# Kernel tuning notes

Measured on AMD Instinct MI355X. Metric: run time of the kernel, lower is better.

The kernel has to match this reference:

```python
import jax, jax.numpy as jnp
import numpy as np

# ---- constants mirroring init_kwargs ----
S = 128          # sheet_units
KA = 25          # aff_cf_units
C = 2            # aff_cf_channels
KL = 25          # lat_cf_units
EXC = 9          # exc_units
DA = 1           # aff_cf_dilation
DL = 1           # lat_cf_dilation
HOMEO_TARGET = 0.04
STRENGTH = 1.0

# ---- radial helper masks (get_circle / get_radial_cos) ----
def _dist(n):
    g = jnp.arange(n, dtype=jnp.float32) - (n - 1) / 2.0
    return jnp.sqrt(g[:, None] ** 2 + g[None, :] ** 2)

def _circle(n, r):
    return (_dist(n) < r).astype(jnp.float32)

def _rcos(n, wl):
    return jnp.cos(_dist(n) * jnp.pi / wl)

# afferent envelope: [C*KA*KA], channel-major like torch repeat+view
_ae = _rcos(KA, KA) ** 2 * _circle(KA, KA / 2)
_ae = _ae / _ae.max()
AFF_ENV = jnp.tile(_ae.reshape(1, KA * KA), (C, 1)).reshape(C * KA * KA)

# lateral (LRI) envelope: [KL*KL]
_inh = _rcos(KL, EXC / DL) ** 2 * _circle(KL, EXC / (2 * DL))
_le = _rcos(KL, KL) ** 2 * (1.0 - _inh) * _circle(KL, KL / 2)
LRI_ENV = (_le / _le.max()).reshape(KL * KL)

def _unfold(x, k, dil):
    """x: [C,H,W] -> patches [L, C*k*k], torch F.unfold ordering (C slowest)."""
    Cc, H, W = x.shape
    out = H - dil * (k - 1)
    idx = jnp.arange(out)[:, None] + dil * jnp.arange(k)[None, :]  # [out,k]
    p = x[:, idx, :]          # [C,out,k,W]
    p = p[:, :, :, idx]       # [C,out,k,out,k]
    p = p.transpose(1, 3, 0, 2, 4)  # [out_i,out_j,C,ki,kj]
    return p.reshape(out * out, Cc * k * k)

def setup_inputs() -> dict:
    key = jax.random.key(0)
    k1, k2 = jax.random.split(key)
    in_size = S + DA * (KA - 1)  # 152
    x = jax.random.uniform(k1, (1, C, in_size, in_size), dtype=jnp.float32)
    rfs = jax.random.uniform(k2, (S * S, C * KA * KA, 1), dtype=jnp.float32)
    rfs = rfs / rfs.sum(1, keepdims=True)
    lat_weights = jnp.ones((S * S, KL * KL, 1), jnp.float32) / (KL * KL)
    adathresh = jnp.zeros((1, 1, S, S), jnp.float32)
    return {"x": x, "rfs": rfs, "lat_weights": lat_weights, "adathresh": adathresh}

def _forward(x, rfs, lat_weights, adathresh):
    relu = jax.nn.relu
    rfs = relu(rfs)                 # no_grad positive clamp of params
    lw = relu(lat_weights)
    # afferent: unfold + envelope + per-pixel dot (bmm with [L,F,1])
    tiles = _unfold(x[0], KA, DA) * AFF_ENV[None, :]          # [L, C*KA*KA]
    raw_aff = jnp.einsum('lf,lf->l', tiles, rfs[:, :, 0]).reshape(S, S)
    aff = jax.lax.stop_gradient(raw_aff) - adathresh[0, 0]
    lat = relu(aff)
    # lateral inhibition: pad so unfold yields S*S positions
    p = DL * (KL - 1) // 2
    lt = _unfold(jnp.pad(lat, p)[None], KL, DL) * LRI_ENV[None, :]  # [L, KL*KL]
    lat_neg = jnp.einsum('lf,lf->l', lt, jax.lax.stop_gradient(lw)[:, :, 0]).reshape(S, S)
    lat = lat - lat_neg
    lat = jnp.tanh(relu(lat * STRENGTH + aff))
    # hebbian lateral correlations term (learning_flag path)
    lt2 = _unfold(jnp.pad(lat, p, constant_values=HOMEO_TARGET)[None], KL, DL) * LRI_ENV[None, :]
    weighted = lt2 * lat.reshape(S * S, 1)
    lat_correlations = jnp.einsum('lf,lf->', weighted, lw[:, :, 0])
    return (raw_aff.reshape(1, 1, S, S), lat.reshape(1, 1, S, S),
            lat_correlations, tiles[:, None, :])

def reference(x, rfs, lat_weights, adathresh):
    return _forward(x, rfs, lat_weights, adathresh)
```

## Files before the change

kernel.cpp:

```cpp
#include <hip/hip_runtime.h>
#include <math.h>

#define S 128
#define KA 25
#define KL 25
#define PATCH (KA * KA)
#define FEAT (2 * PATCH)
#define PI_F 3.14159265358979323846f

#define WS_ENV 0
#define WS_LAT0 640
#define WS_PART 17024

__global__ __launch_bounds__(256) void k_tiles_aff(const float* __restrict__ x,
                                                   const float* __restrict__ rfs,
                                                   const float* __restrict__ ada,
                                                   float* __restrict__ raw_aff,
                                                   float* __restrict__ tiles,
                                                   float* __restrict__ ws) {
    __shared__ float s_ae[PATCH];
    __shared__ float s_part[4];
    const int tid = threadIdx.x;
    const int lane = tid & 63;
    const int wv = tid >> 6;

    for (int i = tid; i < PATCH; i += 256) {
        float di = (float)(i / KA) - 12.0f;
        float dj = (float)(i % KA) - 12.0f;
        float d = sqrtf(di * di + dj * dj);
        float v = 0.0f;
        if (d < 12.5f) {
            float c = cosf(d * (PI_F / 25.0f));
            v = c * c;
        }
        s_ae[i] = v;
    }
    __syncthreads();

    const int l = blockIdx.x;
    const int li = l >> 7;
    const int lj = l & 127;
    const long base = (long)l * FEAT;

    float acc = 0.0f;
    for (int f = tid; f < FEAT; f += 256) {
        int c = (f >= PATCH) ? 1 : 0;
        int r = f - c * PATCH;
        int ki = r / KA;
        int kj = r - ki * KA;
        float xv = x[c * (152 * 152) + (li + ki) * 152 + (lj + kj)];
        float t = xv * s_ae[r];
        tiles[base + f] = t;
        acc += t * fmaxf(rfs[base + f], 0.0f);
    }

    for (int off = 32; off > 0; off >>= 1) acc += __shfl_down(acc, off);
    if (lane == 0) s_part[wv] = acc;
    __syncthreads();
    if (tid == 0) {
        float ra = s_part[0] + s_part[1] + s_part[2] + s_part[3];
        raw_aff[l] = ra;
        ws[WS_LAT0 + l] = fmaxf(ra - ada[l], 0.0f);
    }

    if (blockIdx.x == 0) {
        __syncthreads();
        float m = 0.0f;
        for (int i = tid; i < PATCH; i += 256) {
            float di = (float)(i / KL) - 12.0f;
            float dj = (float)(i % KL) - 12.0f;
            float d = sqrtf(di * di + dj * dj);
            float v = 0.0f;
            if (d < 12.5f) {
                float c1 = cosf(d * (PI_F / 25.0f));
                float inh = 0.0f;
                if (d < 4.5f) {
                    float c2 = cosf(d * (PI_F / 9.0f));
                    inh = c2 * c2;
                }
                v = c1 * c1 * (1.0f - inh);
            }
            s_ae[i] = v;
            m = fmaxf(m, v);
        }
        for (int off = 32; off > 0; off >>= 1) m = fmaxf(m, __shfl_down(m, off));
        if (lane == 0) s_part[wv] = m;
        __syncthreads();
        float inv = 1.0f / fmaxf(fmaxf(s_part[0], s_part[1]),
                                 fmaxf(s_part[2], s_part[3]));
        for (int i = tid; i < PATCH; i += 256) ws[WS_ENV + i] = s_ae[i] * inv;
    }
}

__global__ __launch_bounds__(256) void k_lat(const float* __restrict__ raw_aff,
                                             const float* __restrict__ ada,
                                             const float* __restrict__ lw,
                                             float* __restrict__ latf,
                                             const float* __restrict__ ws) {
    __shared__ float s_le[PATCH];
    const int tid = threadIdx.x;
    for (int i = tid; i < PATCH; i += 256) s_le[i] = ws[WS_ENV + i];
    __syncthreads();

    const int lane = tid & 63;
    const int wv = tid >> 6;
    const int l = blockIdx.x * 4 + wv;
    const int li = l >> 7;
    const int lj = l & 127;
    const long base = (long)l * PATCH;
    const float* __restrict__ lat0 = ws + WS_LAT0;

    float acc = 0.0f;
    for (int f = lane; f < PATCH; f += 64) {
        int ki = f / KL;
        int kj = f - ki * KL;
        int ri = li + ki - 12;
        int rj = lj + kj - 12;
        float lv = 0.0f;
        if (ri >= 0 && ri < S && rj >= 0 && rj < S) lv = lat0[ri * S + rj];
        acc += lv * s_le[f] * fmaxf(lw[base + f], 0.0f);
    }
    for (int off = 32; off > 0; off >>= 1) acc += __shfl_down(acc, off);

    if (lane == 0) {
        float aff_l = raw_aff[l] - ada[l];
        float lat0_l = fmaxf(aff_l, 0.0f);
        float v = (lat0_l - acc)  + aff_l;
        latf[l] = tanhf(fmaxf(v, 0.0f));
    }
}

__global__ __launch_bounds__(256) void k_corr(const float* __restrict__ latf,
                                              const float* __restrict__ lw,
                                              float* __restrict__ ws) {
    __shared__ float s_le[PATCH];
    __shared__ float s_part[4];
    const int tid = threadIdx.x;
    for (int i = tid; i < PATCH; i += 256) s_le[i] = ws[WS_ENV + i];
    __syncthreads();

    const int lane = tid & 63;
    const int wv = tid >> 6;
    const int l = blockIdx.x * 4 + wv;
    const int li = l >> 7;
    const int lj = l & 127;
    const long base = (long)l * PATCH;

    float acc = 0.0f;
    for (int f = lane; f < PATCH; f += 64) {
        int ki = f / KL;
        int kj = f - ki * KL;
        int ri = li + ki - 12;
        int rj = lj + kj - 12;
        float lv = 0.04f;
        if (ri >= 0 && ri < S && rj >= 0 && rj < S) lv = latf[ri * S + rj];
        acc += lv * s_le[f] * fmaxf(lw[base + f], 0.0f);
    }
    for (int off = 32; off > 0; off >>= 1) acc += __shfl_down(acc, off);

    if (lane == 0) s_part[wv] = acc * latf[l];
    __syncthreads();
    if (tid == 0)
        ws[WS_PART + blockIdx.x] = s_part[0] + s_part[1] + s_part[2] + s_part[3];
}

__global__ __launch_bounds__(256) void k_reduce(const float* __restrict__ ws,
                                                float* __restrict__ corr) {
    __shared__ float s_part[4];
    const int tid = threadIdx.x;
    const int lane = tid & 63;
    const int wv = tid >> 6;
    float acc = 0.0f;
    for (int i = tid; i < 4096; i += 256) acc += ws[WS_PART + i];
    for (int off = 32; off > 0; off >>= 1) acc += __shfl_down(acc, off);
    if (lane == 0) s_part[wv] = acc;
    __syncthreads();
    if (tid == 0) corr[0] = s_part[0] + s_part[1] + s_part[2] + s_part[3];
}

extern "C" void kernel_launch(void* const* d_in, const int* in_sizes, int n_in,
                              void* d_out, int out_size, void* d_ws, size_t ws_size,
                              hipStream_t stream) {
    const float* x   = (const float*)d_in[0];
    const float* rfs = (const float*)d_in[1];
    const float* lw  = (const float*)d_in[2];
    const float* ada = (const float*)d_in[3];

    float* out      = (float*)d_out;
    float* raw_aff  = out;
    float* latf     = out + S * S;
    float* corr     = out + 2 * S * S;
    float* tiles    = out + 2 * S * S + 1;
    float* ws       = (float*)d_ws;

    k_tiles_aff<<<S * S, 256, 0, stream>>>(x, rfs, ada, raw_aff, tiles, ws);
    k_lat<<<(S * S) / 4, 256, 0, stream>>>(raw_aff, ada, lw, latf, ws);
    k_corr<<<(S * S) / 4, 256, 0, stream>>>(latf, lw, ws);
    k_reduce<<<1, 256, 0, stream>>>(ws, corr);
}
```

Measured before the change: 229.7 us.

## Split tile output into vectorized kernel, pad lateral maps, vectorize weight loads

Moves the large tiles output write into its own grid-stride kernel that emits aligned float4 stores, and makes the afferent dot-product kernel read rfs as float4 with peel and tail handling. Precomputes both envelopes once in an init kernel, and writes the lateral activity maps into zero- and 0.04-padded 152x152 buffers so the lateral and correlation passes need no bounds checks. Those passes also read lw as float4. The cost is that x is read twice, through two kernel launches, and the padded buffers are re-initialized on every call.

```diff
diff --git a/kernel.cpp b/kernel.cpp
--- a/kernel.cpp
+++ b/kernel.cpp
@@ -4,91 +4,175 @@
 #define S 128
 #define KA 25
 #define KL 25
-#define PATCH (KA * KA)
-#define FEAT (2 * PATCH)
+#define PATCH 625
+#define FEAT 1250
 #define PI_F 3.14159265358979323846f
-
-#define WS_ENV 0
-#define WS_LAT0 640
-#define WS_PART 17024
-
-__global__ __launch_bounds__(256) void k_tiles_aff(const float* __restrict__ x,
-                                                   const float* __restrict__ rfs,
-                                                   const float* __restrict__ ada,
-                                                   float* __restrict__ raw_aff,
-                                                   float* __restrict__ tiles,
-                                                   float* __restrict__ ws) {
-    __shared__ float s_ae[PATCH];
+#define PADW 152
+#define PADA (PADW * PADW)
+
+#define WS_LRI 0
+#define WS_AE 640
+#define WS_LAT0P 1280
+#define WS_LATFP 24384
+#define WS_PART 47488
+
+__device__ __forceinline__ int div25(int r) { return (r * 10486) >> 18; }
+
+__device__ __forceinline__ int woff(int r) { return r + 127 * div25(r); }
+
+__global__ __launch_bounds__(256) void k_init(float* __restrict__ ws) {
+    const int tid = threadIdx.x;
+    if (blockIdx.x == 0) {
+        __shared__ float s_tmp[640];
+        __shared__ float s_red[4];
+        for (int s = tid; s < 640; s += 256) {
+            int q = s / 160;
+            int t = s - q * 160;
+            int r = (t << 2) | q;
+            float v = 0.0f;
+            if (r < PATCH) {
+                float di = (float)div25(r) - 12.0f;
+                float dj = (float)(r - 25 * div25(r)) - 12.0f;
+                float d = sqrtf(di * di + dj * dj);
+                if (d < 12.5f) {
+                    float c = cosf(d * (PI_F / 25.0f));
+                    v = c * c;
+                }
+            }
+            ws[WS_AE + s] = v;
+        }
+        float m = 0.0f;
+        for (int s = tid; s < 640; s += 256) {
+            int q = s / 160;
+            int t = s - q * 160;
+            int r = (t << 2) | q;
+            float v = 0.0f;
+            if (r < PATCH) {
+                float di = (float)div25(r) - 12.0f;
+                float dj = (float)(r - 25 * div25(r)) - 12.0f;
+                float d = sqrtf(di * di + dj * dj);
+                if (d < 12.5f) {
+                    float c1 = cosf(d * (PI_F / 25.0f));
+                    float inh = 0.0f;
+                    if (d < 4.5f) {
+                        float c2 = cosf(d * (PI_F / 9.0f));
+                        inh = c2 * c2;
+                    }
+                    v = c1 * c1 * (1.0f - inh);
+                }
+            }
+            s_tmp[s] = v;
+            m = fmaxf(m, v);
+        }
+        for (int o = 32; o; o >>= 1) m = fmaxf(m, __shfl_down(m, o));
+        if (!(tid & 63)) s_red[tid >> 6] = m;
+        __syncthreads();
+        float inv = 1.0f / fmaxf(fmaxf(s_red[0], s_red[1]),
+                                 fmaxf(s_red[2], s_red[3]));
+        for (int s = tid; s < 640; s += 256) ws[WS_LRI + s] = s_tmp[s] * inv;
+    }
+    const int gid = blockIdx.x * 256 + tid;
+    const int gsz = gridDim.x * 256;
+    for (int i = gid; i < 2 * PADA; i += gsz) {
+        if (i < PADA) ws[WS_LAT0P + i] = 0.0f;
+        else          ws[WS_LATFP + i - PADA] = 0.04f;
+    }
+}
+
+__global__ __launch_bounds__(256) void k_aff(const float* __restrict__ x,
+                                             const float* __restrict__ rfs,
+                                             const float* __restrict__ ada,
+                                             float* __restrict__ raw_aff,
+                                             float* __restrict__ ws) {
+    __shared__ float s_ae[640];
     __shared__ float s_part[4];
     const int tid = threadIdx.x;
-    const int lane = tid & 63;
-    const int wv = tid >> 6;
-
-    for (int i = tid; i < PATCH; i += 256) {
-        float di = (float)(i / KA) - 12.0f;
-        float dj = (float)(i % KA) - 12.0f;
-        float d = sqrtf(di * di + dj * dj);
-        float v = 0.0f;
-        if (d < 12.5f) {
-            float c = cosf(d * (PI_F / 25.0f));
-            v = c * c;
-        }
-        s_ae[i] = v;
-    }
+    for (int i = tid; i < 640; i += 256) s_ae[i] = ws[WS_AE + i];
     __syncthreads();
 
     const int l = blockIdx.x;
     const int li = l >> 7;
     const int lj = l & 127;
+    const int wbase = li * PADW + lj;
     const long base = (long)l * FEAT;
+    const int peel = (l & 1) ? 2 : 0;
 
     float acc = 0.0f;
-    for (int f = tid; f < FEAT; f += 256) {
-        int c = (f >= PATCH) ? 1 : 0;
-        int r = f - c * PATCH;
-        int ki = r / KA;
-        int kj = r - ki * KA;
-        float xv = x[c * (152 * 152) + (li + ki) * 152 + (lj + kj)];
-        float t = xv * s_ae[r];
-        tiles[base + f] = t;
+    if (tid < peel) {
+        int f = tid;
+        float t = x[wbase + f] * s_ae[(f & 3) * 160 + (f >> 2)];
         acc += t * fmaxf(rfs[base + f], 0.0f);
     }
-
-    for (int off = 32; off > 0; off >>= 1) acc += __shfl_down(acc, off);
-    if (lane == 0) s_part[wv] = acc;
-    __syncthreads();
-    if (tid == 0) {
+    const int n4 = (FEAT - peel) >> 2;
+    for (int k = tid; k < n4; k += 256) {
+        int f0 = peel + (k << 2);
+        const float4 rv = *reinterpret_cast<const float4*>(rfs + base + f0);
+#pragma unroll
+        for (int j = 0; j < 4; ++j) {
+            int f = f0 + j;
+            int c = (f >= PATCH);
+            int r = f - (c ? PATCH : 0);
+            float t = x[c * PADA + wbase + woff(r)]
+                      * s_ae[(r & 3) * 160 + (r >> 2)];
+            acc += t * fmaxf((&rv.x)[j], 0.0f);
+        }
+    }
+    const int tail = (FEAT - peel) & 3;
+    if (tid < tail) {
+        int f = peel + (n4 << 2) + tid;
+        int r = f - PATCH;
+        float t = x[PADA + wbase + woff(r)] * s_ae[(r & 3) * 160 + (r >> 2)];
+        acc += t * fmaxf(rfs[base + f], 0.0f);
+    }
+
+    for (int o = 32; o; o >>= 1) acc += __shfl_down(acc, o);
+    const int lane = tid & 63, wv = tid >> 6;
+    if (!lane) s_part[wv] = acc;
+    __syncthreads();
+    if (!tid) {
         float ra = s_part[0] + s_part[1] + s_part[2] + s_part[3];
         raw_aff[l] = ra;
-        ws[WS_LAT0 + l] = fmaxf(ra - ada[l], 0.0f);
-    }
-
-    if (blockIdx.x == 0) {
-        __syncthreads();
-        float m = 0.0f;
-        for (int i = tid; i < PATCH; i += 256) {
-            float di = (float)(i / KL) - 12.0f;
-            float dj = (float)(i % KL) - 12.0f;
-            float d = sqrtf(di * di + dj * dj);
-            float v = 0.0f;
-            if (d < 12.5f) {
-                float c1 = cosf(d * (PI_F / 25.0f));
-                float inh = 0.0f;
-                if (d < 4.5f) {
-                    float c2 = cosf(d * (PI_F / 9.0f));
-                    inh = c2 * c2;
-                }
-                v = c1 * c1 * (1.0f - inh);
-            }
-            s_ae[i] = v;
-            m = fmaxf(m, v);
-        }
-        for (int off = 32; off > 0; off >>= 1) m = fmaxf(m, __shfl_down(m, off));
-        if (lane == 0) s_part[wv] = m;
-        __syncthreads();
-        float inv = 1.0f / fmaxf(fmaxf(s_part[0], s_part[1]),
-                                 fmaxf(s_part[2], s_part[3]));
-        for (int i = tid; i < PATCH; i += 256) ws[WS_ENV + i] = s_ae[i] * inv;
+        ws[WS_LAT0P + (li + 12) * PADW + (lj + 12)] = fmaxf(ra - ada[l], 0.0f);
+    }
+}
+
+#define NTILE 20480000
+#define NF4 5119999
+__global__ __launch_bounds__(256) void k_tiles(const float* __restrict__ x,
+                                               float* __restrict__ tiles,
+                                               const float* __restrict__ ws) {
+    __shared__ float s_ae[640];
+    const int tid = threadIdx.x;
+    for (int i = tid; i < 640; i += 256) s_ae[i] = ws[WS_AE + i];
+    __syncthreads();
+
+    const int gid = blockIdx.x * 256 + tid;
+    const int gsz = gridDim.x * 256;
+    for (long k = gid; k < NF4; k += gsz) {
+        long i0 = 3 + (k << 2);
+        float4 v;
+#pragma unroll
+        for (int j = 0; j < 4; ++j) {
+            unsigned int e = (unsigned int)(i0 + j);
+            unsigned int l = e / 1250u;
+            int f = (int)(e - l * 1250u);
+            int c = (f >= PATCH);
+            int r = f - (c ? PATCH : 0);
+            int li = (int)(l >> 7), lj = (int)(l & 127u);
+            (&v.x)[j] = x[c * PADA + li * PADW + lj + woff(r)]
+                        * s_ae[(r & 3) * 160 + (r >> 2)];
+        }
+        *reinterpret_cast<float4*>(tiles + i0) = v;
+    }
+    if (blockIdx.x == 0 && tid < 4) {
+        unsigned int e = (tid < 3) ? (unsigned int)tid : (NTILE - 1u);
+        unsigned int l = e / 1250u;
+        int f = (int)(e - l * 1250u);
+        int c = (f >= PATCH);
+        int r = f - (c ? PATCH : 0);
+        int li = (int)(l >> 7), lj = (int)(l & 127u);
+        tiles[e] = x[c * PADA + li * PADW + lj + woff(r)]
+                   * s_ae[(r & 3) * 160 + (r >> 2)];
     }
 }
 
@@ -96,71 +180,100 @@
                                              const float* __restrict__ ada,
                                              const float* __restrict__ lw,
                                              float* __restrict__ latf,
-                                             const float* __restrict__ ws) {
-    __shared__ float s_le[PATCH];
-    const int tid = threadIdx.x;
-    for (int i = tid; i < PATCH; i += 256) s_le[i] = ws[WS_ENV + i];
-    __syncthreads();
-
-    const int lane = tid & 63;
-    const int wv = tid >> 6;
+                                             float* __restrict__ ws) {
+    __shared__ float s_le[640];
+    const int tid = threadIdx.x;
+    for (int i = tid; i < 640; i += 256) s_le[i] = ws[WS_LRI + i];
+    __syncthreads();
+
+    const int lane = tid & 63, wv = tid >> 6;
     const int l = blockIdx.x * 4 + wv;
-    const int li = l >> 7;
-    const int lj = l & 127;
+    const int li = l >> 7, lj = l & 127;
+    const int wbase = li * PADW + lj;
     const long base = (long)l * PATCH;
-    const float* __restrict__ lat0 = ws + WS_LAT0;
+    const float* __restrict__ plat0 = ws + WS_LAT0P;
 
     float acc = 0.0f;
-    for (int f = lane; f < PATCH; f += 64) {
-        int ki = f / KL;
-        int kj = f - ki * KL;
-        int ri = li + ki - 12;
-        int rj = lj + kj - 12;
-        float lv = 0.0f;
-        if (ri >= 0 && ri < S && rj >= 0 && rj < S) lv = lat0[ri * S + rj];
-        acc += lv * s_le[f] * fmaxf(lw[base + f], 0.0f);
-    }
-    for (int off = 32; off > 0; off >>= 1) acc += __shfl_down(acc, off);
-
-    if (lane == 0) {
+    const int peel = (4 - (l & 3)) & 3;
+    if (lane < peel) {
+        int f = lane;
+        acc += plat0[wbase + f] * s_le[(f & 3) * 160 + (f >> 2)]
+               * fmaxf(lw[base + f], 0.0f);
+    }
+    const int n4 = (PATCH - peel) >> 2;
+    for (int k = lane; k < n4; k += 64) {
+        int f0 = peel + (k << 2);
+        const float4 w4 = *reinterpret_cast<const float4*>(lw + base + f0);
+#pragma unroll
+        for (int j = 0; j < 4; ++j) {
+            int f = f0 + j;
+            acc += plat0[wbase + woff(f)] * s_le[(f & 3) * 160 + (f >> 2)]
+                   * fmaxf((&w4.x)[j], 0.0f);
+        }
+    }
+    const int tail = (PATCH - peel) & 3;
+    if (lane < tail) {
+        int f = peel + (n4 << 2) + lane;
+        acc += plat0[wbase + woff(f)] * s_le[(f & 3) * 160 + (f >> 2)]
+               * fmaxf(lw[base + f], 0.0f);
+    }
+    for (int o = 32; o; o >>= 1) acc += __shfl_down(acc, o);
+
+    if (!lane) {
         float aff_l = raw_aff[l] - ada[l];
         float lat0_l = fmaxf(aff_l, 0.0f);
         float v = (lat0_l - acc)  + aff_l;
-        latf[l] = tanhf(fmaxf(v, 0.0f));
+        float lv = tanhf(fmaxf(v, 0.0f));
+        latf[l] = lv;
+        ws[WS_LATFP + (li + 12) * PADW + (lj + 12)] = lv;
     }
 }
 
 __global__ __launch_bounds__(256) void k_corr(const float* __restrict__ latf,
                                               const float* __restrict__ lw,
                                               float* __restrict__ ws) {
-    __shared__ float s_le[PATCH];
+    __shared__ float s_le[640];
     __shared__ float s_part[4];
     const int tid = threadIdx.x;
-    for (int i = tid; i < PATCH; i += 256) s_le[i] = ws[WS_ENV + i];
-    __syncthreads();
-
-    const int lane = tid & 63;
-    const int wv = tid >> 6;
+    for (int i = tid; i < 640; i += 256) s_le[i] = ws[WS_LRI + i];
+    __syncthreads();
+
+    const int lane = tid & 63, wv = tid >> 6;
     const int l = blockIdx.x * 4 + wv;
-    const int li = l >> 7;
-    const int lj = l & 127;
+    const int li = l >> 7, lj = l & 127;
+    const int wbase = li * PADW + lj;
     const long base = (long)l * PATCH;
+    const float* __restrict__ platf = ws + WS_LATFP;
 
     float acc = 0.0f;
-    for (int f = lane; f < PATCH; f += 64) {
-        int ki = f / KL;
-        int kj = f - ki * KL;
-        int ri = li + ki - 12;
-        int rj = lj + kj - 12;
-        float lv = 0.04f;
-        if (ri >= 0 && ri < S && rj >= 0 && rj < S) lv = latf[ri * S + rj];
-        acc += lv * s_le[f] * fmaxf(lw[base + f], 0.0f);
-    }
-    for (int off = 32; off > 0; off >>= 1) acc += __shfl_down(acc, off);
-
-    if (lane == 0) s_part[wv] = acc * latf[l];
-    __syncthreads();
-    if (tid == 0)
+    const int peel = (4 - (l & 3)) & 3;
+    if (lane < peel) {
+        int f = lane;
+        acc += platf[wbase + f] * s_le[(f & 3) * 160 + (f >> 2)]
+               * fmaxf(lw[base + f], 0.0f);
+    }
+    const int n4 = (PATCH - peel) >> 2;
+    for (int k = lane; k < n4; k += 64) {
+        int f0 = peel + (k << 2);
+        const float4 w4 = *reinterpret_cast<const float4*>(lw + base + f0);
+#pragma unroll
+        for (int j = 0; j < 4; ++j) {
+            int f = f0 + j;
+            acc += platf[wbase + woff(f)] * s_le[(f & 3) * 160 + (f >> 2)]
+                   * fmaxf((&w4.x)[j], 0.0f);
+        }
+    }
+    const int tail = (PATCH - peel) & 3;
+    if (lane < tail) {
+        int f = peel + (n4 << 2) + lane;
+        acc += platf[wbase + woff(f)] * s_le[(f & 3) * 160 + (f >> 2)]
+               * fmaxf(lw[base + f], 0.0f);
+    }
+    for (int o = 32; o; o >>= 1) acc += __shfl_down(acc, o);
+
+    if (!lane) s_part[wv] = acc * latf[l];
+    __syncthreads();
+    if (!tid)
         ws[WS_PART + blockIdx.x] = s_part[0] + s_part[1] + s_part[2] + s_part[3];
 }
 
@@ -168,14 +281,13 @@
                                                 float* __restrict__ corr) {
     __shared__ float s_part[4];
     const int tid = threadIdx.x;
-    const int lane = tid & 63;
-    const int wv = tid >> 6;
+    const int lane = tid & 63, wv = tid >> 6;
     float acc = 0.0f;
     for (int i = tid; i < 4096; i += 256) acc += ws[WS_PART + i];
-    for (int off = 32; off > 0; off >>= 1) acc += __shfl_down(acc, off);
-    if (lane == 0) s_part[wv] = acc;
-    __syncthreads();
-    if (tid == 0) corr[0] = s_part[0] + s_part[1] + s_part[2] + s_part[3];
+    for (int o = 32; o; o >>= 1) acc += __shfl_down(acc, o);
+    if (!lane) s_part[wv] = acc;
+    __syncthreads();
+    if (!tid) corr[0] = s_part[0] + s_part[1] + s_part[2] + s_part[3];
 }
 
 extern "C" void kernel_launch(void* const* d_in, const int* in_sizes, int n_in,
@@ -193,7 +305,9 @@
     float* tiles    = out + 2 * S * S + 1;
     float* ws       = (float*)d_ws;
 
-    k_tiles_aff<<<S * S, 256, 0, stream>>>(x, rfs, ada, raw_aff, tiles, ws);
+    k_init<<<16, 256, 0, stream>>>(ws);
+    k_aff<<<S * S, 256, 0, stream>>>(x, rfs, ada, raw_aff, ws);
+    k_tiles<<<4096, 256, 0, stream>>>(x, tiles, ws);
     k_lat<<<(S * S) / 4, 256, 0, stream>>>(raw_aff, ada, lw, latf, ws);
     k_corr<<<(S * S) / 4, 256, 0, stream>>>(latf, lw, ws);
     k_reduce<<<1, 256, 0, stream>>>(ws, corr);
```

New measurement: 244.3 us. 6.4% more time.
